# Performance work log

Hardware: AMD Instinct MI355X
Metric: run time of the kernel (lower is better)

## Reference

```python
import jax, jax.numpy as jnp
import numpy as np

N_NODES = 50000
N_EDGES = 800000


def gat_conv(x, src, dst, ea, W, We, a_s, a_d, a_e, b, n_nodes):
    """PyG GATConv with edge_dim, add_self_loops=True, fill_value='mean', concat=True."""
    H, C = a_s.shape
    dt = x.dtype
    # self-loop edge_attr = mean of incoming edge attrs per destination node
    deg = jax.ops.segment_sum(jnp.ones((src.shape[0],), dt), dst, num_segments=n_nodes)
    loop_attr = jax.ops.segment_sum(ea, dst, num_segments=n_nodes) / jnp.clip(deg, 1.0)[:, None]
    nodes = jnp.arange(n_nodes, dtype=src.dtype)
    s = jnp.concatenate([src, nodes])
    d = jnp.concatenate([dst, nodes])
    e_attr = jnp.concatenate([ea, loop_attr], axis=0)       # [E2, edge_dim]
    h = (x @ W).reshape(n_nodes, H, C)                       # [N,H,C]
    e = (e_attr @ We).reshape(-1, H, C)                      # [E2,H,C]
    a_src = jnp.einsum('nhc,hc->nh', h, a_s)                 # [N,H]
    a_dst = jnp.einsum('nhc,hc->nh', h, a_d)
    a_edg = jnp.einsum('ehc,hc->eh', e, a_e)                 # [E2,H]
    lg = jax.nn.leaky_relu(a_src[s] + a_dst[d] + a_edg, 0.2)  # [E2,H]
    m = jax.ops.segment_max(lg, d, num_segments=n_nodes)     # every node has a self-loop
    p = jnp.exp(lg - m[d])
    z = jax.ops.segment_sum(p, d, num_segments=n_nodes)
    alpha = p / z[d]                                         # segment softmax over dst
    out = jax.ops.segment_sum(alpha[:, :, None] * h[s], d, num_segments=n_nodes)
    return out.reshape(n_nodes, H * C) + b


def setup_inputs() -> dict:
    key = jax.random.key(0)
    ks = iter(jax.random.split(key, 40))
    sc = 0.05
    inp = {
        'x': jax.random.normal(next(ks), (N_NODES, 128), jnp.float32),
        'edge_index': jax.random.randint(next(ks), (2, N_EDGES), 0, N_NODES, dtype=jnp.int32),
        'edge_attr': jax.random.uniform(next(ks), (N_EDGES, 1), jnp.float32),
        'fa_w': jax.random.normal(next(ks), (128, 128)) * sc, 'fa_b': jnp.zeros((128,)),
        'W1': jax.random.normal(next(ks), (128, 256)) * sc, 'We1': jax.random.normal(next(ks), (1, 256)) * sc,
        'as1': jax.random.normal(next(ks), (4, 64)) * sc, 'ad1': jax.random.normal(next(ks), (4, 64)) * sc,
        'ae1': jax.random.normal(next(ks), (4, 64)) * sc, 'b1': jnp.zeros((256,)),
        'W2': jax.random.normal(next(ks), (256, 256)) * sc, 'We2': jax.random.normal(next(ks), (1, 256)) * sc,
        'as2': jax.random.normal(next(ks), (4, 64)) * sc, 'ad2': jax.random.normal(next(ks), (4, 64)) * sc,
        'ae2': jax.random.normal(next(ks), (4, 64)) * sc, 'b2': jnp.zeros((256,)),
        'W3': jax.random.normal(next(ks), (256, 64)) * sc, 'We3': jax.random.normal(next(ks), (1, 64)) * sc,
        'as3': jax.random.normal(next(ks), (1, 64)) * sc, 'ad3': jax.random.normal(next(ks), (1, 64)) * sc,
        'ae3': jax.random.normal(next(ks), (1, 64)) * sc, 'b3': jnp.zeros((64,)),
        'r1_w': jax.random.normal(next(ks), (128, 256)) * sc, 'r1_b': jnp.zeros((256,)),
        'r2_w': jax.random.normal(next(ks), (256, 256)) * sc, 'r2_b': jnp.zeros((256,)),
        'ffn_w1': jax.random.normal(next(ks), (128, 64)) * sc, 'ffn_b1': jnp.zeros((64,)),
        'ffn_w2': jax.random.normal(next(ks), (64, 64)) * sc, 'ffn_b2': jnp.zeros((64,)),
    }
    return inp


def reference(x, edge_index, edge_attr, fa_w, fa_b,
              W1, We1, as1, ad1, ae1, b1,
              W2, We2, as2, ad2, ae2, b2,
              W3, We3, as3, ad3, ae3, b3,
              r1_w, r1_b, r2_w, r2_b,
              ffn_w1, ffn_b1, ffn_w2, ffn_b2):
    n = x.shape[0]
    src, dst = edge_index[0], edge_index[1]
    # feature attention gate
    x = x * jax.nn.sigmoid(x @ fa_w + fa_b)
    xr1 = x @ r1_w + r1_b
    z1 = gat_conv(x, src, dst, edge_attr, W1, We1, as1, ad1, ae1, b1, n)
    z1 = jax.nn.leaky_relu(z1, 0.01) + xr1          # dropout = identity (eval)
    z2 = gat_conv(z1, src, dst, edge_attr, W2, We2, as2, ad2, ae2, b2, n)
    z2 = jax.nn.leaky_relu(z2, 0.01) + (z1 @ r2_w + r2_b)
    z3 = gat_conv(z2, src, dst, edge_attr, W3, We3, as3, ad3, ae3, b3, n)
    z_self = jax.nn.relu(x @ ffn_w1 + ffn_b1) @ ffn_w2 + ffn_b2
    z3 = jax.nn.leaky_relu(z3, 0.01) + z_self
    return z3
```

## Files before the change

### kernel.cpp

```cpp
#include <hip/hip_runtime.h>
#include <hip/hip_bf16.h>


typedef unsigned short u16;
typedef unsigned int   u32;
typedef __attribute__((ext_vector_type(8))) short short8;
typedef __attribute__((ext_vector_type(4))) float float4v;

typedef const __attribute__((address_space(1))) u32* gptr_t;
typedef __attribute__((address_space(3))) u32* lptr_t;
#define GLOAD_LDS16(g, l) \
    __builtin_amdgcn_global_load_lds((gptr_t)(const void*)(g), (lptr_t)(void*)(l), 16, 0, 0)

static __device__ __forceinline__ u16 f2b(float f) {
    u32 u = __float_as_uint(f);
    u32 r = u + 0x7fffu + ((u >> 16) & 1u);
    return (u16)(r >> 16);
}
static __device__ __forceinline__ float b2f(u16 u) {
    return __uint_as_float(((u32)u) << 16);
}
static __device__ __forceinline__ float lo2f(u32 v) { return __uint_as_float(v << 16); }
static __device__ __forceinline__ float hi2f(u32 v) { return __uint_as_float(v & 0xffff0000u); }
static __device__ __forceinline__ float lrelu02(float x) { return fmaxf(x, 0.2f * x); }

__global__ void prep_mega(const float* __restrict__ x, u16* __restrict__ xb, int n4,
                          const float* s0, const float* s1, const float* s2,
                          const float* s3, const float* s4, const float* s5,
                          const float* s6, const float* s7,
                          u16* d0, u16* d1, u16* d2, u16* d3,
                          u16* d4, u16* d5, u16* d6, u16* d7,
                          const float* We1, const float* ae1,
                          const float* We2, const float* ae2,
                          const float* We3, const float* ae3, float* ce_g,
                          const int* __restrict__ ei,
                          u32* deg, u32* rank, int E) {
    int role = blockIdx.y;
    if (role == 0) {
        int i = blockIdx.x * 256 + threadIdx.x;
        if (i >= n4) return;
        float4 v = ((const float4*)x)[i];
        ushort4 o;
        o.x = f2b(v.x); o.y = f2b(v.y); o.z = f2b(v.z); o.w = f2b(v.w);
        ((ushort4*)xb)[i] = o;
    } else if (role == 2) {
        int e = blockIdx.x * 256 + threadIdx.x;
        if (e >= E) return;
        int d = ei[E + e];
        rank[e] = atomicAdd(&deg[d], 1u);
    } else {
        int wid = blockIdx.x >> 4, sub = blockIdx.x & 15;
        if (wid > 8) return;
        if (wid == 8) {
            if (sub == 0) {
                int t = threadIdx.x;
                if (t < 9) {
                    const float* W; const float* a; int h;
                    if (t < 4)      { W = We1; a = ae1; h = t; }
                    else if (t < 8) { W = We2; a = ae2; h = t - 4; }
                    else            { W = We3; a = ae3; h = 0; }
                    float s = 0.f;
                    for (int c = 0; c < 64; c++) s += W[h * 64 + c] * a[h * 64 + c];
                    ce_g[t] = s;
                }
            }
            return;
        }
        const float* src; u16* dst; int K, N;
        switch (wid) {
            case 0: src = s0; dst = d0; K = 128; N = 128; break;
            case 1: src = s1; dst = d1; K = 128; N = 256; break;
            case 2: src = s2; dst = d2; K = 128; N = 256; break;
            case 3: src = s3; dst = d3; K = 256; N = 256; break;
            case 4: src = s4; dst = d4; K = 256; N = 256; break;
            case 5: src = s5; dst = d5; K = 256; N = 64;  break;
            case 6: src = s6; dst = d6; K = 128; N = 64;  break;
            default: src = s7; dst = d7; K = 64;  N = 64;  break;
        }
        int KN = K * N;
        int nmask = N - 1;
        int nshift = __popc((u32)nmask);
        for (int i = sub * 256 + threadIdx.x; i < KN; i += 16 * 256) {
            int k = i >> nshift, n2 = i & nmask;
            dst[(size_t)n2 * K + k] = f2b(src[i]);
        }
    }
}

__global__ void scan_block_kernel(const u32* __restrict__ deg, int* incl,
                                  int* blocksum, int Nn) {
    __shared__ int sb[256];
    int t = threadIdx.x;
    int n = blockIdx.x * 256 + t;
    int v = (n < Nn) ? (int)deg[n] : 0;
    sb[t] = v;
    __syncthreads();
    for (int off = 1; off < 256; off <<= 1) {
        int x = (t >= off) ? sb[t - off] : 0;
        __syncthreads();
        sb[t] += x;
        __syncthreads();
    }
    if (n < Nn) incl[n] = sb[t];
    if (t == 255) blocksum[blockIdx.x] = sb[255];
}

__global__ void scan_final_kernel(const u32* __restrict__ deg, const int* __restrict__ incl,
                                  const int* __restrict__ blocksum,
                                  int* row_ptr, int Nn) {
    __shared__ int sb[256];
    int t = threadIdx.x;
    int b = blockIdx.x;
    sb[t] = (t < b) ? blocksum[t] : 0;
    __syncthreads();
    for (int off = 128; off > 0; off >>= 1) {
        if (t < off) sb[t] += sb[t + off];
        __syncthreads();
    }
    int base = sb[0];
    int n = b * 256 + t;
    if (n >= Nn) return;
    int d = (int)deg[n];
    int excl = base + incl[n] - d;
    row_ptr[n] = excl;
    if (n == Nn - 1) row_ptr[Nn] = excl + d;
}

__global__ void scatter_kernel(const int* __restrict__ ei, const float* __restrict__ ea,
                               const int* __restrict__ row_ptr, const u32* __restrict__ rank,
                               int2* __restrict__ csr2, int E) {
    int e = blockIdx.x * 256 + threadIdx.x;
    if (e >= E) return;
    int d = ei[E + e];
    int pos = row_ptr[d] + (int)rank[e];
    csr2[pos] = make_int2(ei[e], __float_as_int(ea[e]));
}

template <int EPI, int K>
__global__ __launch_bounds__(256)
void gemm128_kernel(const u16* __restrict__ A, const u16* __restrict__ Bt,
                    const float* __restrict__ bias,
                    float* __restrict__ Cf, u16* __restrict__ Cb, int N) {
    __shared__ u16 As[128 * 32];
    __shared__ u16 Bs[128 * 32];
    int t = threadIdx.x;
    int w = t >> 6, lane = t & 63;
    int wm = w & 1, wn = w >> 1;
    int lm = lane & 15, q = lane >> 4;
    int bm = blockIdx.x * 128, bn = blockIdx.y * 128;

    float4v acc[4][4];
#pragma unroll
    for (int i = 0; i < 4; i++)
#pragma unroll
        for (int j = 0; j < 4; j++) acc[i][j] = (float4v){0.f, 0.f, 0.f, 0.f};

    int srow = lane >> 2;
    int scol = (lane & 3) * 8;
    const u16* aG = A + (size_t)(bm + w * 32 + srow) * K + scol;
    const u16* bG = Bt + (size_t)(bn + w * 32 + srow) * K + scol;
    u16* aL0 = &As[(w * 32) * 32];
    u16* aL1 = &As[(w * 32 + 16) * 32];
    u16* bL0 = &Bs[(w * 32) * 32];
    u16* bL1 = &Bs[(w * 32 + 16) * 32];

#pragma unroll
    for (int k0 = 0; k0 < K; k0 += 32) {
        GLOAD_LDS16(aG + k0, aL0);
        GLOAD_LDS16(aG + (size_t)16 * K + k0, aL1);
        GLOAD_LDS16(bG + k0, bL0);
        GLOAD_LDS16(bG + (size_t)16 * K + k0, bL1);
        __syncthreads();

        short8 af[4], bf[4];
#pragma unroll
        for (int i = 0; i < 4; i++)
            af[i] = *(const short8*)&As[(64 * wm + 16 * i + lm) * 32 + q * 8];
#pragma unroll
        for (int j = 0; j < 4; j++)
            bf[j] = *(const short8*)&Bs[(64 * wn + 16 * j + lm) * 32 + q * 8];
#pragma unroll
        for (int i = 0; i < 4; i++)
#pragma unroll
            for (int j = 0; j < 4; j++)
                acc[i][j] = __builtin_amdgcn_mfma_f32_16x16x32_bf16(af[i], bf[j], acc[i][j], 0, 0, 0);
        __syncthreads();
    }

#pragma unroll
    for (int i = 0; i < 4; i++)
#pragma unroll
        for (int j = 0; j < 4; j++) {
            int col = bn + 64 * wn + 16 * j + lm;
#pragma unroll
            for (int r = 0; r < 4; r++) {
                int row = bm + 64 * wm + 16 * i + q * 4 + r;
                float v = acc[i][j][r];
                if (EPI == 4) {
                    if (col < 256) {
                        v += bias[col];
                        Cf[(size_t)row * 256 + col] = v;
                    } else {
                        Cb[(size_t)row * 256 + (col - 256)] = f2b(v);
                    }
                } else {
                    Cb[(size_t)row * N + col] = f2b(v);
                }
            }
        }
}

template <int EPI, int K>
__global__ __launch_bounds__(256)
void gemm_kernel(const u16* __restrict__ A, const u16* __restrict__ Bt,
                 const float* __restrict__ bias, const u16* __restrict__ extraB,
                 float* __restrict__ Cf, u16* __restrict__ Cb, int N) {
#define LDSS 40
    __shared__ u16 As[64 * LDSS];
    __shared__ u16 Bs[64 * LDSS];
    int t = threadIdx.x;
    int bm = blockIdx.x * 64, bn = blockIdx.y * 64;
    int w = t >> 6, lane = t & 63;
    int wm = w & 1, wn = w >> 1;
    int lm = lane & 15, q = lane >> 4;

    float4v acc[2][2];
#pragma unroll
    for (int i = 0; i < 2; i++)
#pragma unroll
        for (int j = 0; j < 2; j++) acc[i][j] = (float4v){0.f, 0.f, 0.f, 0.f};

    int ar = t >> 2;
    int ac = (t & 3) * 8;
    const u16* aPtr = A + (size_t)(bm + ar) * K + ac;
    const u16* bPtr = Bt + (size_t)(bn + ar) * K + ac;

#pragma unroll
    for (int k0 = 0; k0 < K; k0 += 32) {
        uint4 av = *(const uint4*)(aPtr + k0);
        uint4 bv = *(const uint4*)(bPtr + k0);
        *(uint4*)&As[ar * LDSS + ac] = av;
        *(uint4*)&Bs[ar * LDSS + ac] = bv;
        __syncthreads();

        short8 fa0 = *(const short8*)&As[(32 * wm + lm) * LDSS + q * 8];
        short8 fa1 = *(const short8*)&As[(32 * wm + 16 + lm) * LDSS + q * 8];
        short8 fb0 = *(const short8*)&Bs[(32 * wn + lm) * LDSS + q * 8];
        short8 fb1 = *(const short8*)&Bs[(32 * wn + 16 + lm) * LDSS + q * 8];
        acc[0][0] = __builtin_amdgcn_mfma_f32_16x16x32_bf16(fa0, fb0, acc[0][0], 0, 0, 0);
        acc[0][1] = __builtin_amdgcn_mfma_f32_16x16x32_bf16(fa0, fb1, acc[0][1], 0, 0, 0);
        acc[1][0] = __builtin_amdgcn_mfma_f32_16x16x32_bf16(fa1, fb0, acc[1][0], 0, 0, 0);
        acc[1][1] = __builtin_amdgcn_mfma_f32_16x16x32_bf16(fa1, fb1, acc[1][1], 0, 0, 0);
        __syncthreads();
    }

#pragma unroll
    for (int i = 0; i < 2; i++)
#pragma unroll
        for (int j = 0; j < 2; j++) {
            int col = bn + 32 * wn + 16 * j + lm;
            float bval = (EPI >= 1) ? bias[col] : 0.f;
#pragma unroll
            for (int r = 0; r < 4; r++) {
                int row = bm + 32 * wm + 16 * i + q * 4 + r;
                float v = acc[i][j][r] + bval;
                if (EPI == 2) v = fmaxf(v, 0.f);
                if (EPI == 3) {
                    float xv = b2f(extraB[(size_t)row * N + col]);
                    v = xv / (1.f + __expf(-v));
                }
                size_t o = (size_t)row * N + col;
                if (EPI == 1) Cf[o] = v;
                else Cb[o] = f2b(v);
            }
        }
}

__global__ __launch_bounds__(256)
void att4_kernel(const uint2* __restrict__ hb2, const float* __restrict__ a_s,
                 const float* __restrict__ a_d, float* att_s, float* att_d, int Nn) {
    int wv = threadIdx.x >> 6;
    int n = blockIdx.x * 4 + wv;
    if (n >= Nn) return;
    int lane = threadIdx.x & 63;
    float4 as4 = *(const float4*)&a_s[lane * 4];
    float4 ad4 = *(const float4*)&a_d[lane * 4];
    uint2 v = hb2[(size_t)n * 64 + lane];
    float c0 = lo2f(v.x), c1 = hi2f(v.x), c2 = lo2f(v.y), c3 = hi2f(v.y);
    float ps = c0 * as4.x + c1 * as4.y + c2 * as4.z + c3 * as4.w;
    float pd = c0 * ad4.x + c1 * ad4.y + c2 * ad4.z + c3 * ad4.w;
#pragma unroll
    for (int off = 8; off > 0; off >>= 1) {
        ps += __shfl_down(ps, off);
        pd += __shfl_down(pd, off);
    }
    if ((lane & 15) == 0) {
        att_s[n * 4 + (lane >> 4)] = ps;
        att_d[n * 4 + (lane >> 4)] = pd;
    }
}

__global__ __launch_bounds__(256)
void att1_kernel(const u32* __restrict__ hb, const float* __restrict__ a_s,
                 const float* __restrict__ a_d, float* att_s, float* att_d, int Nn) {
    int wv = threadIdx.x >> 6;
    int n = blockIdx.x * 4 + wv;
    if (n >= Nn) return;
    int lane = threadIdx.x & 63;
    int cl = lane & 31;
    float2 as2 = *(const float2*)&a_s[cl * 2];
    float2 ad2 = *(const float2*)&a_d[cl * 2];
    u32 v = hb[(u32)n * 32u + cl];
    float c0 = lo2f(v), c1 = hi2f(v);
    float ps = c0 * as2.x + c1 * as2.y;
    float pd = c0 * ad2.x + c1 * ad2.y;
    if (lane >= 32) { ps = 0.f; pd = 0.f; }
#pragma unroll
    for (int off = 16; off > 0; off >>= 1) {
        ps += __shfl_down(ps, off);
        pd += __shfl_down(pd, off);
    }
    if (lane == 0) {
        att_s[n] = ps;
        att_d[n] = pd;
    }
}

__global__ __launch_bounds__(256)
void agg4_kernel(const uint2* __restrict__ hb2,
                 const float* __restrict__ att_s, const float* __restrict__ att_d,
                 const int* __restrict__ row_ptr, const int2* __restrict__ csr2,
                 const float* __restrict__ ce_g, const float* __restrict__ bias,
                 const float* __restrict__ resid, u16* __restrict__ outb, int Nn) {
    int wv = __builtin_amdgcn_readfirstlane(threadIdx.x >> 6);
    int n = blockIdx.x * 4 + wv;
    if (n >= Nn) return;
    int lane = threadIdx.x & 63;
    int hh = lane >> 4;

    float ce = ce_g[hh];
    float adn = att_d[n * 4 + hh];
    float asn = att_s[n * 4 + hh];
    uint2 sv = hb2[(size_t)n * 64 + lane];
    float z = 0.f, qsum = 0.f;
    float aA0 = 0.f, aA1 = 0.f, aA2 = 0.f, aA3 = 0.f;
    float aB0 = 0.f, aB1 = 0.f, aB2 = 0.f, aB3 = 0.f;

    int e0 = row_ptr[n], e1 = row_ptr[n + 1];
    for (int base = e0; base < e1; base += 64) {
        int cnt = min(64, e1 - base);
        int2 cc = csr2[base + min(lane, cnt - 1)];
        int vsrc = cc.x;
        float vea = __int_as_float(cc.y);
        int i = 0;
        for (; i + 8 <= cnt; i += 8) {
            int s0 = __shfl(vsrc, i),     s1 = __shfl(vsrc, i + 1);
            int s2 = __shfl(vsrc, i + 2), s3 = __shfl(vsrc, i + 3);
            int s4 = __shfl(vsrc, i + 4), s5 = __shfl(vsrc, i + 5);
            int s6 = __shfl(vsrc, i + 6), s7 = __shfl(vsrc, i + 7);
            float q0 = __shfl(vea, i),     q1 = __shfl(vea, i + 1);
            float q2 = __shfl(vea, i + 2), q3 = __shfl(vea, i + 3);
            float q4 = __shfl(vea, i + 4), q5 = __shfl(vea, i + 5);
            float q6 = __shfl(vea, i + 6), q7 = __shfl(vea, i + 7);
            float g0 = att_s[(u32)s0 * 4u + hh], g1 = att_s[(u32)s1 * 4u + hh];
            float g2 = att_s[(u32)s2 * 4u + hh], g3 = att_s[(u32)s3 * 4u + hh];
            float g4 = att_s[(u32)s4 * 4u + hh], g5 = att_s[(u32)s5 * 4u + hh];
            float g6 = att_s[(u32)s6 * 4u + hh], g7 = att_s[(u32)s7 * 4u + hh];
            uint2 v0 = hb2[(u32)s0 * 64u + lane], v1 = hb2[(u32)s1 * 64u + lane];
            uint2 v2 = hb2[(u32)s2 * 64u + lane], v3 = hb2[(u32)s3 * 64u + lane];
            uint2 v4 = hb2[(u32)s4 * 64u + lane], v5 = hb2[(u32)s5 * 64u + lane];
            uint2 v6 = hb2[(u32)s6 * 64u + lane], v7 = hb2[(u32)s7 * 64u + lane];
            float p0 = __expf(lrelu02(g0 + adn + q0 * ce));
            float p1 = __expf(lrelu02(g1 + adn + q1 * ce));
            float p2 = __expf(lrelu02(g2 + adn + q2 * ce));
            float p3 = __expf(lrelu02(g3 + adn + q3 * ce));
            float p4 = __expf(lrelu02(g4 + adn + q4 * ce));
            float p5 = __expf(lrelu02(g5 + adn + q5 * ce));
            float p6 = __expf(lrelu02(g6 + adn + q6 * ce));
            float p7 = __expf(lrelu02(g7 + adn + q7 * ce));
            qsum += ((q0 + q1) + (q2 + q3)) + ((q4 + q5) + (q6 + q7));
            z += ((p0 + p1) + (p2 + p3)) + ((p4 + p5) + (p6 + p7));
            aA0 = fmaf(p0, lo2f(v0.x), aA0); aA1 = fmaf(p0, hi2f(v0.x), aA1);
            aA2 = fmaf(p0, lo2f(v0.y), aA2); aA3 = fmaf(p0, hi2f(v0.y), aA3);
            aB0 = fmaf(p1, lo2f(v1.x), aB0); aB1 = fmaf(p1, hi2f(v1.x), aB1);
            aB2 = fmaf(p1, lo2f(v1.y), aB2); aB3 = fmaf(p1, hi2f(v1.y), aB3);
            aA0 = fmaf(p2, lo2f(v2.x), aA0); aA1 = fmaf(p2, hi2f(v2.x), aA1);
            aA2 = fmaf(p2, lo2f(v2.y), aA2); aA3 = fmaf(p2, hi2f(v2.y), aA3);
            aB0 = fmaf(p3, lo2f(v3.x), aB0); aB1 = fmaf(p3, hi2f(v3.x), aB1);
            aB2 = fmaf(p3, lo2f(v3.y), aB2); aB3 = fmaf(p3, hi2f(v3.y), aB3);
            aA0 = fmaf(p4, lo2f(v4.x), aA0); aA1 = fmaf(p4, hi2f(v4.x), aA1);
            aA2 = fmaf(p4, lo2f(v4.y), aA2); aA3 = fmaf(p4, hi2f(v4.y), aA3);
            aB0 = fmaf(p5, lo2f(v5.x), aB0); aB1 = fmaf(p5, hi2f(v5.x), aB1);
            aB2 = fmaf(p5, lo2f(v5.y), aB2); aB3 = fmaf(p5, hi2f(v5.y), aB3);
            aA0 = fmaf(p6, lo2f(v6.x), aA0); aA1 = fmaf(p6, hi2f(v6.x), aA1);
            aA2 = fmaf(p6, lo2f(v6.y), aA2); aA3 = fmaf(p6, hi2f(v6.y), aA3);
            aB0 = fmaf(p7, lo2f(v7.x), aB0); aB1 = fmaf(p7, hi2f(v7.x), aB1);
            aB2 = fmaf(p7, lo2f(v7.y), aB2); aB3 = fmaf(p7, hi2f(v7.y), aB3);
        }
        for (; i < cnt; i++) {
            int s = __shfl(vsrc, i);
            float q = __shfl(vea, i);
            float g = att_s[(u32)s * 4u + hh];
            uint2 v = hb2[(u32)s * 64u + lane];
            float p = __expf(lrelu02(g + adn + q * ce));
            qsum += q;
            z += p;
            aA0 = fmaf(p, lo2f(v.x), aA0); aA1 = fmaf(p, hi2f(v.x), aA1);
            aA2 = fmaf(p, lo2f(v.y), aA2); aA3 = fmaf(p, hi2f(v.y), aA3);
        }
    }
    float la = qsum / (float)max(e1 - e0, 1);
    float ps = __expf(lrelu02(asn + adn + la * ce));
    z += ps;
    float a0 = aA0 + aB0 + ps * lo2f(sv.x);
    float a1 = aA1 + aB1 + ps * hi2f(sv.x);
    float a2 = aA2 + aB2 + ps * lo2f(sv.y);
    float a3 = aA3 + aB3 + ps * hi2f(sv.y);

    float inv = 1.f / z;
    int c0 = lane * 4;
    float4 bv = *(const float4*)&bias[c0];
    float4 rv = *(const float4*)&resid[(size_t)n * 256 + c0];
    float o0 = fmaf(a0, inv, bv.x);
    float o1 = fmaf(a1, inv, bv.y);
    float o2 = fmaf(a2, inv, bv.z);
    float o3 = fmaf(a3, inv, bv.w);
    o0 = fmaxf(o0, 0.01f * o0) + rv.x;
    o1 = fmaxf(o1, 0.01f * o1) + rv.y;
    o2 = fmaxf(o2, 0.01f * o2) + rv.z;
    o3 = fmaxf(o3, 0.01f * o3) + rv.w;
    uint2 packed;
    packed.x = ((u32)f2b(o0)) | (((u32)f2b(o1)) << 16);
    packed.y = ((u32)f2b(o2)) | (((u32)f2b(o3)) << 16);
    ((uint2*)outb)[(size_t)n * 64 + lane] = packed;
}

__global__ __launch_bounds__(256)
void agg1_kernel(const uint2* __restrict__ hb2,
                 const float* __restrict__ att_s, const float* __restrict__ att_d,
                 const int* __restrict__ row_ptr, const int2* __restrict__ csr2,
                 const float* __restrict__ ce_g, const float* __restrict__ bias,
                 const float* __restrict__ resid, float* __restrict__ outf, int Nn) {
    int wv = __builtin_amdgcn_readfirstlane(threadIdx.x >> 6);
    int n = blockIdx.x * 4 + wv;
    if (n >= Nn) return;
    int lane = threadIdx.x & 63;
    int qtr = lane >> 4;
    int cl = lane & 15;

    float ce = ce_g[8];
    float adn = att_d[n];
    float asn = att_s[n];
    uint2 sv = hb2[(u32)n * 16u + cl];
    float z = 0.f, qsum = 0.f;
    float a0 = 0.f, a1 = 0.f, a2 = 0.f, a3 = 0.f;

    int e0 = row_ptr[n], e1 = row_ptr[n + 1];
    for (int base = e0; base < e1; base += 64) {
        int cnt = min(64, e1 - base);
        int2 cc = csr2[base + min(lane, cnt - 1)];
        int vsrc = cc.x;
        float vea = __int_as_float(cc.y);
        for (int i = 0; i < cnt; i += 4) {
            int idx = min(i + qtr, cnt - 1);
            int s = __shfl(vsrc, idx);
            float q = __shfl(vea, idx);
            bool act = (i + qtr < cnt);
            float p = __expf(lrelu02(att_s[s] + adn + q * ce));
            p = act ? p : 0.f;
            q = act ? q : 0.f;
            uint2 v = hb2[(u32)s * 16u + cl];
            z += p;
            qsum += q;
            a0 = fmaf(p, lo2f(v.x), a0);
            a1 = fmaf(p, hi2f(v.x), a1);
            a2 = fmaf(p, lo2f(v.y), a2);
            a3 = fmaf(p, hi2f(v.y), a3);
        }
    }
    z += __shfl_xor(z, 16);      z += __shfl_xor(z, 32);
    qsum += __shfl_xor(qsum, 16); qsum += __shfl_xor(qsum, 32);
    a0 += __shfl_xor(a0, 16);    a0 += __shfl_xor(a0, 32);
    a1 += __shfl_xor(a1, 16);    a1 += __shfl_xor(a1, 32);
    a2 += __shfl_xor(a2, 16);    a2 += __shfl_xor(a2, 32);
    a3 += __shfl_xor(a3, 16);    a3 += __shfl_xor(a3, 32);

    float la = qsum / (float)max(e1 - e0, 1);
    float ps = __expf(lrelu02(asn + adn + la * ce));
    z += ps;
    a0 += ps * lo2f(sv.x);
    a1 += ps * hi2f(sv.x);
    a2 += ps * lo2f(sv.y);
    a3 += ps * hi2f(sv.y);

    if (lane < 16) {
        float inv = 1.f / z;
        int c0 = cl * 4;
        float4 bv = *(const float4*)&bias[c0];
        float4 rv = *(const float4*)&resid[(size_t)n * 64 + c0];
        float o0 = fmaf(a0, inv, bv.x);
        float o1 = fmaf(a1, inv, bv.y);
        float o2 = fmaf(a2, inv, bv.z);
        float o3 = fmaf(a3, inv, bv.w);
        o0 = fmaxf(o0, 0.01f * o0) + rv.x;
        o1 = fmaxf(o1, 0.01f * o1) + rv.y;
        o2 = fmaxf(o2, 0.01f * o2) + rv.z;
        o3 = fmaxf(o3, 0.01f * o3) + rv.w;
        *(float4*)&outf[(size_t)n * 64 + c0] = make_float4(o0, o1, o2, o3);
    }
}

extern "C" void kernel_launch(void* const* d_in, const int* in_sizes, int n_in,
                              void* d_out, int out_size, void* d_ws, size_t ws_size,
                              hipStream_t stream) {
    const float* x    = (const float*)d_in[0];
    const int*   ei   = (const int*)d_in[1];
    const float* ea   = (const float*)d_in[2];
    const float* fa_w = (const float*)d_in[3];
    const float* fa_b = (const float*)d_in[4];
    const float* W1   = (const float*)d_in[5];
    const float* We1  = (const float*)d_in[6];
    const float* as1  = (const float*)d_in[7];
    const float* ad1  = (const float*)d_in[8];
    const float* ae1  = (const float*)d_in[9];
    const float* b1   = (const float*)d_in[10];
    const float* W2   = (const float*)d_in[11];
    const float* We2  = (const float*)d_in[12];
    const float* as2  = (const float*)d_in[13];
    const float* ad2  = (const float*)d_in[14];
    const float* ae2  = (const float*)d_in[15];
    const float* b2   = (const float*)d_in[16];
    const float* W3   = (const float*)d_in[17];
    const float* We3  = (const float*)d_in[18];
    const float* as3  = (const float*)d_in[19];
    const float* ad3  = (const float*)d_in[20];
    const float* ae3  = (const float*)d_in[21];
    const float* b3   = (const float*)d_in[22];
    const float* r1_w = (const float*)d_in[23];
    const float* r1_b = (const float*)d_in[24];
    const float* r2_w = (const float*)d_in[25];
    const float* r2_b = (const float*)d_in[26];
    const float* fw1  = (const float*)d_in[27];
    const float* fb1  = (const float*)d_in[28];
    const float* fw2  = (const float*)d_in[29];
    const float* fb2  = (const float*)d_in[30];

    const int Nn = in_sizes[0] / 128;
    const int E  = in_sizes[1] / 2;

    char* ws = (char*)d_ws;
    size_t off = 0;
    auto alloc = [&](size_t bytes) -> char* {
        char* p = ws + off;
        off += (bytes + 255) & ~((size_t)255);
        return p;
    };
    u32*   deg      = (u32*)alloc((size_t)Nn * 4);
    u32*   rank     = (u32*)alloc((size_t)E * 4);
    int*   incl     = (int*)alloc((size_t)Nn * 4);
    int*   row_ptr  = (int*)alloc((size_t)(Nn + 1) * 4);
    int*   blocksum = (int*)alloc(1024);
    float* att_s    = (float*)alloc((size_t)Nn * 16);
    float* att_d    = (float*)alloc((size_t)Nn * 16);
    int2*  csr2     = (int2*)alloc((size_t)E * 8);
    float* ce_g     = (float*)alloc(64);
    u16* xbf   = (u16*)alloc((size_t)(Nn + 128) * 128 * 2);
    u16* xg_bf = (u16*)alloc((size_t)(Nn + 128) * 128 * 2);
    u16* h_bf  = (u16*)alloc((size_t)(Nn + 128) * 256 * 2);
    u16* z_bf  = (u16*)alloc((size_t)(Nn + 128) * 256 * 2);
    u16* mid_bf = (u16*)alloc((size_t)(Nn + 128) * 64 * 2);
    u16* h3_bf  = (u16*)alloc((size_t)(Nn + 128) * 64 * 2);
    u16* wt_fa = (u16*)alloc(16384 * 2);
    u16* wt_c1 = (u16*)alloc((size_t)512 * 128 * 2);
    u16* wt_c2 = (u16*)alloc((size_t)512 * 256 * 2);
    u16* wt_W3 = (u16*)alloc(16384 * 2);
    u16* wt_f1 = (u16*)alloc(8192 * 2);
    u16* wt_f2 = (u16*)alloc(4096 * 2);
    float* residB = (float*)alloc((size_t)(Nn + 128) * 256 * 4);
    float* zself  = (float*)alloc((size_t)(Nn + 128) * 64 * 4);

    hipMemsetAsync(deg, 0, (size_t)Nn * 4, stream);

    int eb = (E + 255) / 256;
    int nb = (Nn + 255) / 256;
    int n4 = Nn * 128 / 4;
    int xb4 = (n4 + 255) / 256;

    prep_mega<<<dim3(max(xb4, eb), 3), 256, 0, stream>>>(
        x, xbf, n4,
        fa_w, r1_w, W1, r2_w, W2, W3, fw1, fw2,
        wt_fa, wt_c1, wt_c1 + (size_t)256 * 128, wt_c2, wt_c2 + (size_t)256 * 256,
        wt_W3, wt_f1, wt_f2, We1, ae1, We2, ae2, We3, ae3, ce_g,
        ei, deg, rank, E);
    scan_block_kernel<<<nb, 256, 0, stream>>>(deg, incl, blocksum, Nn);
    scan_final_kernel<<<nb, 256, 0, stream>>>(deg, incl, blocksum, row_ptr, Nn);
    scatter_kernel<<<eb, 256, 0, stream>>>(ei, ea, row_ptr, rank, csr2, E);

    int mb  = (Nn + 63) / 64;
    int mb1 = (Nn + 127) / 128;
    int ab  = (Nn + 3) / 4;

    gemm_kernel<3, 128><<<dim3(mb, 2), 256, 0, stream>>>(xbf, wt_fa, fa_b, xbf, nullptr, xg_bf, 128);
    gemm128_kernel<4, 128><<<dim3(mb1, 4), 256, 0, stream>>>(xg_bf, wt_c1, r1_b, residB, h_bf, 512);
    att4_kernel<<<ab, 256, 0, stream>>>((const uint2*)h_bf, as1, ad1, att_s, att_d, Nn);
    agg4_kernel<<<ab, 256, 0, stream>>>((const uint2*)h_bf, att_s, att_d, row_ptr, csr2,
                                        ce_g, b1, residB, z_bf, Nn);
    gemm128_kernel<4, 256><<<dim3(mb1, 4), 256, 0, stream>>>(z_bf, wt_c2, r2_b, residB, h_bf, 512);
    att4_kernel<<<ab, 256, 0, stream>>>((const uint2*)h_bf, as2, ad2, att_s, att_d, Nn);
    agg4_kernel<<<ab, 256, 0, stream>>>((const uint2*)h_bf, att_s, att_d, row_ptr, csr2,
                                        ce_g + 4, b2, residB, z_bf, Nn);
    gemm_kernel<2, 128><<<dim3(mb, 1), 256, 0, stream>>>(xg_bf, wt_f1, fb1, nullptr, nullptr, mid_bf, 64);
    gemm_kernel<1, 64><<<dim3(mb, 1), 256, 0, stream>>>(mid_bf, wt_f2, fb2, nullptr, zself, nullptr, 64);
    gemm_kernel<0, 256><<<dim3(mb, 1), 256, 0, stream>>>(z_bf, wt_W3, nullptr, nullptr, nullptr, h3_bf, 64);
    att1_kernel<<<ab, 256, 0, stream>>>((const u32*)h3_bf, as3, ad3, att_s, att_d, Nn);
    agg1_kernel<<<ab, 256, 0, stream>>>((const uint2*)h3_bf, att_s, att_d, row_ptr, csr2,
                                        ce_g, b3, zself, (float*)d_out, Nn);
}
```

Baseline: 490.3 us.

## Fuse attention-score projections into GEMM epilogues and shrink agg unroll

Removes the separate att4/att1 kernels by computing per-head source and destination attention dot products directly from the fp32 MFMA accumulators in the GEMM epilogues, using shuffle reductions and, in the small GEMM, an LDS combine across warps. This saves three launches and a re-read of the bf16 h features, and the scores now come from unrounded fp32 values. It also cuts the agg4 gather loop unroll from 8 to 4, lowering register pressure at the cost of fewer loads in flight. The att buffers are padded so padded GEMM rows stay in bounds.

```diff
diff --git a/kernel.cpp b/kernel.cpp
--- a/kernel.cpp
+++ b/kernel.cpp
@@ -140,7 +140,9 @@
 __global__ __launch_bounds__(256)
 void gemm128_kernel(const u16* __restrict__ A, const u16* __restrict__ Bt,
                     const float* __restrict__ bias,
-                    float* __restrict__ Cf, u16* __restrict__ Cb, int N) {
+                    float* __restrict__ Cf, u16* __restrict__ Cb,
+                    const float* __restrict__ a_s, const float* __restrict__ a_d,
+                    float* __restrict__ att_s, float* __restrict__ att_d, int Nn) {
     __shared__ u16 As[128 * 32];
     __shared__ u16 Bs[128 * 32];
     int t = threadIdx.x;
@@ -187,6 +189,7 @@
         __syncthreads();
     }
 
+    bool hside = (EPI == 5) && (blockIdx.y >= 2);
 #pragma unroll
     for (int i = 0; i < 4; i++)
 #pragma unroll
@@ -196,28 +199,58 @@
             for (int r = 0; r < 4; r++) {
                 int row = bm + 64 * wm + 16 * i + q * 4 + r;
                 float v = acc[i][j][r];
-                if (EPI == 4) {
-                    if (col < 256) {
+                if (EPI == 5) {
+                    if (!hside) {
                         v += bias[col];
                         Cf[(size_t)row * 256 + col] = v;
                     } else {
                         Cb[(size_t)row * 256 + (col - 256)] = f2b(v);
                     }
-                } else {
-                    Cb[(size_t)row * N + col] = f2b(v);
                 }
             }
         }
+
+    if (hside) {
+        int head = 2 * ((int)blockIdx.y - 2) + wn;
+        float as4[4], ad4[4];
+#pragma unroll
+        for (int j = 0; j < 4; j++) {
+            as4[j] = a_s[head * 64 + 16 * j + lm];
+            ad4[j] = a_d[head * 64 + 16 * j + lm];
+        }
+#pragma unroll
+        for (int i = 0; i < 4; i++)
+#pragma unroll
+            for (int r = 0; r < 4; r++) {
+                float ps = acc[i][0][r] * as4[0] + acc[i][1][r] * as4[1] +
+                           acc[i][2][r] * as4[2] + acc[i][3][r] * as4[3];
+                float pd = acc[i][0][r] * ad4[0] + acc[i][1][r] * ad4[1] +
+                           acc[i][2][r] * ad4[2] + acc[i][3][r] * ad4[3];
+#pragma unroll
+                for (int off = 8; off > 0; off >>= 1) {
+                    ps += __shfl_down(ps, off);
+                    pd += __shfl_down(pd, off);
+                }
+                int row = bm + 64 * wm + 16 * i + q * 4 + r;
+                if (lm == 0 && row < Nn) {
+                    att_s[row * 4 + head] = ps;
+                    att_d[row * 4 + head] = pd;
+                }
+            }
+    }
 }
 
 template <int EPI, int K>
 __global__ __launch_bounds__(256)
 void gemm_kernel(const u16* __restrict__ A, const u16* __restrict__ Bt,
                  const float* __restrict__ bias, const u16* __restrict__ extraB,
-                 float* __restrict__ Cf, u16* __restrict__ Cb, int N) {
+                 float* __restrict__ Cf, u16* __restrict__ Cb,
+                 const float* __restrict__ a_s, const float* __restrict__ a_d,
+                 float* __restrict__ att_s, float* __restrict__ att_d, int Nn, int N) {
 #define LDSS 40
     __shared__ u16 As[64 * LDSS];
     __shared__ u16 Bs[64 * LDSS];
+    __shared__ float sps[64], spd[64];
     int t = threadIdx.x;
     int bm = blockIdx.x * 64, bn = blockIdx.y * 64;
     int w = t >> 6, lane = t & 63;
@@ -259,7 +292,7 @@
 #pragma unroll
         for (int j = 0; j < 2; j++) {
             int col = bn + 32 * wn + 16 * j + lm;
-            float bval = (EPI >= 1) ? bias[col] : 0.f;
+            float bval = (EPI == 1 || EPI == 2 || EPI == 3) ? bias[col] : 0.f;
 #pragma unroll
             for (int r = 0; r < 4; r++) {
                 int row = bm + 32 * wm + 16 * i + q * 4 + r;
@@ -274,55 +307,53 @@
                 else Cb[o] = f2b(v);
             }
         }
-}
-
-__global__ __launch_bounds__(256)
-void att4_kernel(const uint2* __restrict__ hb2, const float* __restrict__ a_s,
-                 const float* __restrict__ a_d, float* att_s, float* att_d, int Nn) {
-    int wv = threadIdx.x >> 6;
-    int n = blockIdx.x * 4 + wv;
-    if (n >= Nn) return;
-    int lane = threadIdx.x & 63;
-    float4 as4 = *(const float4*)&a_s[lane * 4];
-    float4 ad4 = *(const float4*)&a_d[lane * 4];
-    uint2 v = hb2[(size_t)n * 64 + lane];
-    float c0 = lo2f(v.x), c1 = hi2f(v.x), c2 = lo2f(v.y), c3 = hi2f(v.y);
-    float ps = c0 * as4.x + c1 * as4.y + c2 * as4.z + c3 * as4.w;
-    float pd = c0 * ad4.x + c1 * ad4.y + c2 * ad4.z + c3 * ad4.w;
-#pragma unroll
-    for (int off = 8; off > 0; off >>= 1) {
-        ps += __shfl_down(ps, off);
-        pd += __shfl_down(pd, off);
-    }
-    if ((lane & 15) == 0) {
-        att_s[n * 4 + (lane >> 4)] = ps;
-        att_d[n * 4 + (lane >> 4)] = pd;
-    }
-}
-
-__global__ __launch_bounds__(256)
-void att1_kernel(const u32* __restrict__ hb, const float* __restrict__ a_s,
-                 const float* __restrict__ a_d, float* att_s, float* att_d, int Nn) {
-    int wv = threadIdx.x >> 6;
-    int n = blockIdx.x * 4 + wv;
-    if (n >= Nn) return;
-    int lane = threadIdx.x & 63;
-    int cl = lane & 31;
-    float2 as2 = *(const float2*)&a_s[cl * 2];
-    float2 ad2 = *(const float2*)&a_d[cl * 2];
-    u32 v = hb[(u32)n * 32u + cl];
-    float c0 = lo2f(v), c1 = hi2f(v);
-    float ps = c0 * as2.x + c1 * as2.y;
-    float pd = c0 * ad2.x + c1 * ad2.y;
-    if (lane >= 32) { ps = 0.f; pd = 0.f; }
-#pragma unroll
-    for (int off = 16; off > 0; off >>= 1) {
-        ps += __shfl_down(ps, off);
-        pd += __shfl_down(pd, off);
-    }
-    if (lane == 0) {
-        att_s[n] = ps;
-        att_d[n] = pd;
+
+    if (EPI == 5) {
+        float as2[2], ad2[2];
+#pragma unroll
+        for (int j = 0; j < 2; j++) {
+            as2[j] = a_s[32 * wn + 16 * j + lm];
+            ad2[j] = a_d[32 * wn + 16 * j + lm];
+        }
+        float psv[8], pdv[8];
+#pragma unroll
+        for (int i = 0; i < 2; i++)
+#pragma unroll
+            for (int r = 0; r < 4; r++) {
+                float ps = acc[i][0][r] * as2[0] + acc[i][1][r] * as2[1];
+                float pd = acc[i][0][r] * ad2[0] + acc[i][1][r] * ad2[1];
+#pragma unroll
+                for (int off = 8; off > 0; off >>= 1) {
+                    ps += __shfl_down(ps, off);
+                    pd += __shfl_down(pd, off);
+                }
+                psv[i * 4 + r] = ps;
+                pdv[i * 4 + r] = pd;
+            }
+        if (wn == 0 && lm == 0) {
+#pragma unroll
+            for (int i = 0; i < 2; i++)
+#pragma unroll
+                for (int r = 0; r < 4; r++) {
+                    int rib = 32 * wm + 16 * i + 4 * q + r;
+                    sps[rib] = psv[i * 4 + r];
+                    spd[rib] = pdv[i * 4 + r];
+                }
+        }
+        __syncthreads();
+        if (wn == 1 && lm == 0) {
+#pragma unroll
+            for (int i = 0; i < 2; i++)
+#pragma unroll
+                for (int r = 0; r < 4; r++) {
+                    int rib = 32 * wm + 16 * i + 4 * q + r;
+                    int row = bm + rib;
+                    if (row < Nn) {
+                        att_s[row] = psv[i * 4 + r] + sps[rib];
+                        att_d[row] = pdv[i * 4 + r] + spd[rib];
+                    }
+                }
+        }
     }
 }
 
@@ -353,49 +384,29 @@
         int vsrc = cc.x;
         float vea = __int_as_float(cc.y);
         int i = 0;
-        for (; i + 8 <= cnt; i += 8) {
-            int s0 = __shfl(vsrc, i),     s1 = __shfl(vsrc, i + 1);
-            int s2 = __shfl(vsrc, i + 2), s3 = __shfl(vsrc, i + 3);
-            int s4 = __shfl(vsrc, i + 4), s5 = __shfl(vsrc, i + 5);
-            int s6 = __shfl(vsrc, i + 6), s7 = __shfl(vsrc, i + 7);
-            float q0 = __shfl(vea, i),     q1 = __shfl(vea, i + 1);
-            float q2 = __shfl(vea, i + 2), q3 = __shfl(vea, i + 3);
-            float q4 = __shfl(vea, i + 4), q5 = __shfl(vea, i + 5);
-            float q6 = __shfl(vea, i + 6), q7 = __shfl(vea, i + 7);
-            float g0 = att_s[(u32)s0 * 4u + hh], g1 = att_s[(u32)s1 * 4u + hh];
-            float g2 = att_s[(u32)s2 * 4u + hh], g3 = att_s[(u32)s3 * 4u + hh];
-            float g4 = att_s[(u32)s4 * 4u + hh], g5 = att_s[(u32)s5 * 4u + hh];
-            float g6 = att_s[(u32)s6 * 4u + hh], g7 = att_s[(u32)s7 * 4u + hh];
-            uint2 v0 = hb2[(u32)s0 * 64u + lane], v1 = hb2[(u32)s1 * 64u + lane];
-            uint2 v2 = hb2[(u32)s2 * 64u + lane], v3 = hb2[(u32)s3 * 64u + lane];
-            uint2 v4 = hb2[(u32)s4 * 64u + lane], v5 = hb2[(u32)s5 * 64u + lane];
-            uint2 v6 = hb2[(u32)s6 * 64u + lane], v7 = hb2[(u32)s7 * 64u + lane];
-            float p0 = __expf(lrelu02(g0 + adn + q0 * ce));
-            float p1 = __expf(lrelu02(g1 + adn + q1 * ce));
-            float p2 = __expf(lrelu02(g2 + adn + q2 * ce));
-            float p3 = __expf(lrelu02(g3 + adn + q3 * ce));
-            float p4 = __expf(lrelu02(g4 + adn + q4 * ce));
-            float p5 = __expf(lrelu02(g5 + adn + q5 * ce));
-            float p6 = __expf(lrelu02(g6 + adn + q6 * ce));
-            float p7 = __expf(lrelu02(g7 + adn + q7 * ce));
-            qsum += ((q0 + q1) + (q2 + q3)) + ((q4 + q5) + (q6 + q7));
-            z += ((p0 + p1) + (p2 + p3)) + ((p4 + p5) + (p6 + p7));
-            aA0 = fmaf(p0, lo2f(v0.x), aA0); aA1 = fmaf(p0, hi2f(v0.x), aA1);
-            aA2 = fmaf(p0, lo2f(v0.y), aA2); aA3 = fmaf(p0, hi2f(v0.y), aA3);
-            aB0 = fmaf(p1, lo2f(v1.x), aB0); aB1 = fmaf(p1, hi2f(v1.x), aB1);
-            aB2 = fmaf(p1, lo2f(v1.y), aB2); aB3 = fmaf(p1, hi2f(v1.y), aB3);
-            aA0 = fmaf(p2, lo2f(v2.x), aA0); aA1 = fmaf(p2, hi2f(v2.x), aA1);
-            aA2 = fmaf(p2, lo2f(v2.y), aA2); aA3 = fmaf(p2, hi2f(v2.y), aA3);
-            aB0 = fmaf(p3, lo2f(v3.x), aB0); aB1 = fmaf(p3, hi2f(v3.x), aB1);
-            aB2 = fmaf(p3, lo2f(v3.y), aB2); aB3 = fmaf(p3, hi2f(v3.y), aB3);
-            aA0 = fmaf(p4, lo2f(v4.x), aA0); aA1 = fmaf(p4, hi2f(v4.x), aA1);
-            aA2 = fmaf(p4, lo2f(v4.y), aA2); aA3 = fmaf(p4, hi2f(v4.y), aA3);
-            aB0 = fmaf(p5, lo2f(v5.x), aB0); aB1 = fmaf(p5, hi2f(v5.x), aB1);
-            aB2 = fmaf(p5, lo2f(v5.y), aB2); aB3 = fmaf(p5, hi2f(v5.y), aB3);
-            aA0 = fmaf(p6, lo2f(v6.x), aA0); aA1 = fmaf(p6, hi2f(v6.x), aA1);
-            aA2 = fmaf(p6, lo2f(v6.y), aA2); aA3 = fmaf(p6, hi2f(v6.y), aA3);
-            aB0 = fmaf(p7, lo2f(v7.x), aB0); aB1 = fmaf(p7, hi2f(v7.x), aB1);
-            aB2 = fmaf(p7, lo2f(v7.y), aB2); aB3 = fmaf(p7, hi2f(v7.y), aB3);
+        for (; i + 4 <= cnt; i += 4) {
+            int sA = __shfl(vsrc, i),     sB = __shfl(vsrc, i + 1);
+            int sC = __shfl(vsrc, i + 2), sD = __shfl(vsrc, i + 3);
+            float qA = __shfl(vea, i),     qB = __shfl(vea, i + 1);
+            float qC = __shfl(vea, i + 2), qD = __shfl(vea, i + 3);
+            float gA = att_s[(u32)sA * 4u + hh], gB = att_s[(u32)sB * 4u + hh];
+            float gC = att_s[(u32)sC * 4u + hh], gD = att_s[(u32)sD * 4u + hh];
+            uint2 vA = hb2[(u32)sA * 64u + lane], vB = hb2[(u32)sB * 64u + lane];
+            uint2 vC = hb2[(u32)sC * 64u + lane], vD = hb2[(u32)sD * 64u + lane];
+            float pA = __expf(lrelu02(gA + adn + qA * ce));
+            float pB = __expf(lrelu02(gB + adn + qB * ce));
+            float pC = __expf(lrelu02(gC + adn + qC * ce));
+            float pD = __expf(lrelu02(gD + adn + qD * ce));
+            qsum += (qA + qB) + (qC + qD);
+            z += (pA + pB) + (pC + pD);
+            aA0 = fmaf(pA, lo2f(vA.x), aA0); aA1 = fmaf(pA, hi2f(vA.x), aA1);
+            aA2 = fmaf(pA, lo2f(vA.y), aA2); aA3 = fmaf(pA, hi2f(vA.y), aA3);
+            aB0 = fmaf(pB, lo2f(vB.x), aB0); aB1 = fmaf(pB, hi2f(vB.x), aB1);
+            aB2 = fmaf(pB, lo2f(vB.y), aB2); aB3 = fmaf(pB, hi2f(vB.y), aB3);
+            aA0 = fmaf(pC, lo2f(vC.x), aA0); aA1 = fmaf(pC, hi2f(vC.x), aA1);
+            aA2 = fmaf(pC, lo2f(vC.y), aA2); aA3 = fmaf(pC, hi2f(vC.y), aA3);
+            aB0 = fmaf(pD, lo2f(vD.x), aB0); aB1 = fmaf(pD, hi2f(vD.x), aB1);
+            aB2 = fmaf(pD, lo2f(vD.y), aB2); aB3 = fmaf(pD, hi2f(vD.y), aB3);
         }
         for (; i < cnt; i++) {
             int s = __shfl(vsrc, i);
@@ -478,12 +489,12 @@
             a3 = fmaf(p, hi2f(v.y), a3);
         }
     }
-    z += __shfl_xor(z, 16);      z += __shfl_xor(z, 32);
+    z += __shfl_xor(z, 16);       z += __shfl_xor(z, 32);
     qsum += __shfl_xor(qsum, 16); qsum += __shfl_xor(qsum, 32);
-    a0 += __shfl_xor(a0, 16);    a0 += __shfl_xor(a0, 32);
-    a1 += __shfl_xor(a1, 16);    a1 += __shfl_xor(a1, 32);
-    a2 += __shfl_xor(a2, 16);    a2 += __shfl_xor(a2, 32);
-    a3 += __shfl_xor(a3, 16);    a3 += __shfl_xor(a3, 32);
+    a0 += __shfl_xor(a0, 16);     a0 += __shfl_xor(a0, 32);
+    a1 += __shfl_xor(a1, 16);     a1 += __shfl_xor(a1, 32);
+    a2 += __shfl_xor(a2, 16);     a2 += __shfl_xor(a2, 32);
+    a3 += __shfl_xor(a3, 16);     a3 += __shfl_xor(a3, 32);
 
     float la = qsum / (float)max(e1 - e0, 1);
     float ps = __expf(lrelu02(asn + adn + la * ce));
@@ -560,8 +571,8 @@
     int*   incl     = (int*)alloc((size_t)Nn * 4);
     int*   row_ptr  = (int*)alloc((size_t)(Nn + 1) * 4);
     int*   blocksum = (int*)alloc(1024);
-    float* att_s    = (float*)alloc((size_t)Nn * 16);
-    float* att_d    = (float*)alloc((size_t)Nn * 16);
+    float* att_s    = (float*)alloc((size_t)(Nn + 128) * 16);
+    float* att_d    = (float*)alloc((size_t)(Nn + 128) * 16);
     int2*  csr2     = (int2*)alloc((size_t)E * 8);
     float* ce_g     = (float*)alloc(64);
     u16* xbf   = (u16*)alloc((size_t)(Nn + 128) * 128 * 2);
@@ -600,19 +611,22 @@
     int mb1 = (Nn + 127) / 128;
     int ab  = (Nn + 3) / 4;
 
-    gemm_kernel<3, 128><<<dim3(mb, 2), 256, 0, stream>>>(xbf, wt_fa, fa_b, xbf, nullptr, xg_bf, 128);
-    gemm128_kernel<4, 128><<<dim3(mb1, 4), 256, 0, stream>>>(xg_bf, wt_c1, r1_b, residB, h_bf, 512);
-    att4_kernel<<<ab, 256, 0, stream>>>((const uint2*)h_bf, as1, ad1, att_s, att_d, Nn);
+    gemm_kernel<3, 128><<<dim3(mb, 2), 256, 0, stream>>>(
+        xbf, wt_fa, fa_b, xbf, nullptr, xg_bf, nullptr, nullptr, nullptr, nullptr, Nn, 128);
+    gemm128_kernel<5, 128><<<dim3(mb1, 4), 256, 0, stream>>>(
+        xg_bf, wt_c1, r1_b, residB, h_bf, as1, ad1, att_s, att_d, Nn);
     agg4_kernel<<<ab, 256, 0, stream>>>((const uint2*)h_bf, att_s, att_d, row_ptr, csr2,
                                         ce_g, b1, residB, z_bf, Nn);
-    gemm128_kernel<4, 256><<<dim3(mb1, 4), 256, 0, stream>>>(z_bf, wt_c2, r2_b, residB, h_bf, 512);
-    att4_kernel<<<ab, 256, 0, stream>>>((const uint2*)h_bf, as2, ad2, att_s, att_d, Nn);
+    gemm128_kernel<5, 256><<<dim3(mb1, 4), 256, 0, stream>>>(
+        z_bf, wt_c2, r2_b, residB, h_bf, as2, ad2, att_s, att_d, Nn);
     agg4_kernel<<<ab, 256, 0, stream>>>((const uint2*)h_bf, att_s, att_d, row_ptr, csr2,
                                         ce_g + 4, b2, residB, z_bf, Nn);
-    gemm_kernel<2, 128><<<dim3(mb, 1), 256, 0, stream>>>(xg_bf, wt_f1, fb1, nullptr, nullptr, mid_bf, 64);
-    gemm_kernel<1, 64><<<dim3(mb, 1), 256, 0, stream>>>(mid_bf, wt_f2, fb2, nullptr, zself, nullptr, 64);
-    gemm_kernel<0, 256><<<dim3(mb, 1), 256, 0, stream>>>(z_bf, wt_W3, nullptr, nullptr, nullptr, h3_bf, 64);
-    att1_kernel<<<ab, 256, 0, stream>>>((const u32*)h3_bf, as3, ad3, att_s, att_d, Nn);
+    gemm_kernel<2, 128><<<dim3(mb, 1), 256, 0, stream>>>(
+        xg_bf, wt_f1, fb1, nullptr, nullptr, mid_bf, nullptr, nullptr, nullptr, nullptr, Nn, 64);
+    gemm_kernel<1, 64><<<dim3(mb, 1), 256, 0, stream>>>(
+        mid_bf, wt_f2, fb2, nullptr, zself, nullptr, nullptr, nullptr, nullptr, nullptr, Nn, 64);
+    gemm_kernel<5, 256><<<dim3(mb, 1), 256, 0, stream>>>(
+        z_bf, wt_W3, nullptr, nullptr, nullptr, h3_bf, as3, ad3, att_s, att_d, Nn, 64);
     agg1_kernel<<<ab, 256, 0, stream>>>((const uint2*)h3_bf, att_s, att_d, row_ptr, csr2,
                                         ce_g, b3, zself, (float*)d_out, Nn);
 }
```

After: 510.6 us. +4.1%, slower.
